# Kernel optimization log

Measured on AMD Instinct MI355X. Metric: run time of the kernel, lower is better.

## Reference

```python
import jax, jax.numpy as jnp
import numpy as np

N = 50000      # nodes
E = 800000     # edges (before self-loops)
F_IN = 128     # num_features
HID = 32       # hidden_channels
HEADS = 4
CLS = 40       # num_classes
NEG_SLOPE = 0.2


def setup_inputs() -> dict:
    key = jax.random.key(0)
    ks = jax.random.split(key, 10)
    s = 0.1
    x = jax.random.normal(ks[0], (N, F_IN), jnp.float32)
    edge_index = jax.random.randint(ks[1], (2, E), 0, N, jnp.int32)
    W1 = jax.random.normal(ks[2], (F_IN, HEADS * HID), jnp.float32) * s
    att_src1 = jax.random.normal(ks[3], (HEADS, HID), jnp.float32) * s
    att_dst1 = jax.random.normal(ks[4], (HEADS, HID), jnp.float32) * s
    b1 = jnp.zeros((HEADS * HID,), jnp.float32)
    W2 = jax.random.normal(ks[5], (HEADS * HID, CLS), jnp.float32) * s
    att_src2 = jax.random.normal(ks[6], (1, CLS), jnp.float32) * s
    att_dst2 = jax.random.normal(ks[7], (1, CLS), jnp.float32) * s
    b2 = jnp.zeros((CLS,), jnp.float32)
    return {"x": x, "edge_index": edge_index,
            "W1": W1, "att_src1": att_src1, "att_dst1": att_dst1, "b1": b1,
            "W2": W2, "att_src2": att_src2, "att_dst2": att_dst2, "b2": b2}


def gat_layer(x, src, dst, W, a_src, a_dst, b, concat):
    """PyG GATConv: per-head linear, edge attention logits a_src.h_j + a_dst.h_i,
    LeakyReLU, segment softmax over incoming edges per dst, weighted scatter-sum."""
    n = x.shape[0]
    H, C = a_src.shape
    h = (x @ W).reshape(n, H, C)                       # [N, H, C]
    al_s = jnp.einsum('nhc,hc->nh', h, a_src)          # [N, H]
    al_d = jnp.einsum('nhc,hc->nh', h, a_dst)          # [N, H]
    e = jax.nn.leaky_relu(al_s[src] + al_d[dst], NEG_SLOPE)  # [E, H]
    e_max = jax.lax.stop_gradient(jax.ops.segment_max(e, dst, num_segments=n))
    e = jnp.exp(e - e_max[dst])
    denom = jax.ops.segment_sum(e, dst, num_segments=n)      # [N, H]
    alpha = e / (denom[dst] + 1e-16)                         # [E, H]
    out = jax.ops.segment_sum(h[src] * alpha[:, :, None], dst, num_segments=n)  # [N, H, C]
    out = out.reshape(n, H * C) if concat else out.mean(axis=1)
    return out + b


def reference(x, edge_index, W1, att_src1, att_dst1, b1, W2, att_src2, att_dst2, b2):
    n = x.shape[0]
    loops = jnp.arange(n, dtype=edge_index.dtype)
    src = jnp.concatenate([edge_index[0], loops])  # PyG adds self-loops by default
    dst = jnp.concatenate([edge_index[1], loops])
    h = gat_layer(x, src, dst, W1, att_src1, att_dst1, b1, concat=True)
    h = jax.nn.relu(h)  # dropout is identity in eval mode
    h = gat_layer(h, src, dst, W2, att_src2, att_dst2, b2, concat=False)
    return jax.nn.log_softmax(h, axis=1)
```

## Files before the change

kernel.cpp:

```cpp
#include <hip/hip_runtime.h>
#include <hip/hip_bf16.h>
#include <cstdint>
#include <cstddef>

#define NN 50000
#define EE 800000
#define ETOT (EE + NN)
#define FIN 128
#define D1 128
#define HEADS 4
#define HID 32
#define CLS 40
#define NEG 0.2f
#define MAXDEG 64
#define NPART 8
#define PSIZE 6250
#define GB 104

typedef __attribute__((ext_vector_type(8))) short short8;
typedef __attribute__((ext_vector_type(4))) float float4v;

union U16 { uint4 u; short8 s; };

__device__ __forceinline__ float bf2f(unsigned short u) {
    union { unsigned int i; float f; } v; v.i = ((unsigned int)u) << 16; return v.f;
}
__device__ __forceinline__ unsigned short f2bf(float f) {
    union { unsigned int i; float f; } v; v.f = f;
    unsigned int r = v.i + 0x7fffu + ((v.i >> 16) & 1u);
    return (unsigned short)(r >> 16);
}

__global__ __launch_bounds__(256) void build_k(const int* __restrict__ eidx,
                                               int* __restrict__ cnt,
                                               unsigned short* __restrict__ ssrcp) {
    int part = blockIdx.x & (NPART - 1);
    int g    = blockIdx.x >> 3;
    int lo = part * PSIZE, hi = lo + PSIZE;
    int stride = GB * 256;
    for (int t = g * 256 + (int)threadIdx.x; t < ETOT; t += stride) {
        int dN = (t < EE) ? eidx[EE + t] : (t - EE);
        if (dN >= lo && dN < hi) {
            int sN = (t < EE) ? eidx[t] : dN;
            int slot = atomicAdd(&cnt[dN], 1);
            if (slot < MAXDEG) ssrcp[dN * MAXDEG + slot] = (unsigned short)sN;
        }
    }
}

__global__ __launch_bounds__(256) void gemm1_k(const float* __restrict__ X,
                                               const float* __restrict__ W,
                                               unsigned int* __restrict__ H1b) {
    __shared__ uint4 Wl[2048];
    int t = threadIdx.x;
    for (int g = t; g < 2048; g += 256) {
        int ct = g >> 8, rem = g & 255, kc = rem >> 6, l = rem & 63;
        int c = ct * 16 + (l & 15);
        int k0 = kc * 32 + (l >> 4) * 8;
        U16 u;
#pragma unroll
        for (int j = 0; j < 8; j++) u.s[j] = (short)f2bf(W[(k0 + j) * D1 + c]);
        Wl[g] = u.u;
    }
    __syncthreads();

    int wid = t >> 6, lane = t & 63, quad = lane >> 4, lrow = lane & 15;
    int wrow0 = blockIdx.x * 128 + wid * 32;

    short8 afr[2][4];
#pragma unroll
    for (int rt = 0; rt < 2; rt++) {
        int r = wrow0 + rt * 16 + lrow;
#pragma unroll
        for (int kc = 0; kc < 4; kc++) {
            short8 a = {0, 0, 0, 0, 0, 0, 0, 0};
            if (r < NN) {
                const float* xp = X + (size_t)r * FIN + kc * 32 + quad * 8;
                float4 x0 = *(const float4*)xp;
                float4 x1 = *(const float4*)(xp + 4);
                a[0] = (short)f2bf(x0.x); a[1] = (short)f2bf(x0.y);
                a[2] = (short)f2bf(x0.z); a[3] = (short)f2bf(x0.w);
                a[4] = (short)f2bf(x1.x); a[5] = (short)f2bf(x1.y);
                a[6] = (short)f2bf(x1.z); a[7] = (short)f2bf(x1.w);
            }
            afr[rt][kc] = a;
        }
    }

    float4v acc[2][8];
#pragma unroll
    for (int rt = 0; rt < 2; rt++)
#pragma unroll
        for (int ct = 0; ct < 8; ct++) acc[rt][ct] = (float4v)(0.f);

#pragma unroll
    for (int ct = 0; ct < 8; ct++) {
#pragma unroll
        for (int kc = 0; kc < 4; kc++) {
            U16 b; b.u = Wl[(ct * 4 + kc) * 64 + lane];
            acc[0][ct] = __builtin_amdgcn_mfma_f32_16x16x32_bf16(afr[0][kc], b.s, acc[0][ct], 0, 0, 0);
            acc[1][ct] = __builtin_amdgcn_mfma_f32_16x16x32_bf16(afr[1][kc], b.s, acc[1][ct], 0, 0, 0);
        }
    }

#pragma unroll
    for (int rt = 0; rt < 2; rt++)
#pragma unroll
        for (int ct = 0; ct < 8; ct++)
#pragma unroll
            for (int reg = 0; reg < 4; reg++) {
                float v = acc[rt][ct][reg];
                float o = __shfl_xor(v, 1);
                int r = wrow0 + rt * 16 + quad * 4 + reg;
                if (((lane & 1) == 0) && r < NN) {
                    unsigned int u = (unsigned int)f2bf(v) | ((unsigned int)f2bf(o) << 16);
                    H1b[(size_t)r * 64 + ct * 8 + (lrow >> 1)] = u;
                }
            }
}

__global__ void att1_k(const unsigned int* __restrict__ H1b,
                       const float* __restrict__ a_s, const float* __restrict__ a_d,
                       float* __restrict__ ALS, float* __restrict__ ALD) {
    int t = blockIdx.x * blockDim.x + threadIdx.x;
    if (t >= NN * HEADS) return;
    int n = t >> 2, h = t & 3;
    const unsigned int* row = H1b + (size_t)n * 64 + h * 16;
    float as = 0.f, ad = 0.f;
#pragma unroll
    for (int i = 0; i < 16; i++) {
        unsigned int u = row[i];
        float c0 = bf2f((unsigned short)(u & 0xffffu));
        float c1 = bf2f((unsigned short)(u >> 16));
        as += c0 * a_s[h * HID + 2 * i] + c1 * a_s[h * HID + 2 * i + 1];
        ad += c0 * a_d[h * HID + 2 * i] + c1 * a_d[h * HID + 2 * i + 1];
    }
    ALS[t] = as; ALD[t] = ad;
}

__global__ __launch_bounds__(128) void gather1_k(const int* __restrict__ cnt,
                                                 const unsigned short* __restrict__ ssrcp,
                                                 const unsigned int* __restrict__ H1b,
                                                 const float4* __restrict__ ALS,
                                                 const float4* __restrict__ ALD,
                                                 const float* __restrict__ b1,
                                                 unsigned int* __restrict__ OUT1b) {
    int v = blockIdx.x;
    int t = threadIdx.x;
    int deg = min(cnt[v], MAXDEG);
    __shared__ float w[MAXDEG][4];
    __shared__ int sid[MAXDEG];
    __shared__ float part[4][D1];
    __shared__ float sden[4];
    float4 ad = ALD[v];
    if (t < deg) {
        int s = (int)ssrcp[v * MAXDEG + t];
        sid[t] = s;
        float4 as = ALS[s];
        float l0 = as.x + ad.x; l0 = l0 > 0.f ? l0 : NEG * l0;
        float l1 = as.y + ad.y; l1 = l1 > 0.f ? l1 : NEG * l1;
        float l2 = as.z + ad.z; l2 = l2 > 0.f ? l2 : NEG * l2;
        float l3 = as.w + ad.w; l3 = l3 > 0.f ? l3 : NEG * l3;
        w[t][0] = __expf(l0); w[t][1] = __expf(l1);
        w[t][2] = __expf(l2); w[t][3] = __expf(l3);
    }
    __syncthreads();
    if (t < 4) {
        float d = 0.f;
        for (int j = 0; j < deg; j++) d += w[j][t];
        sden[t] = d;
    }
    int g = t >> 5, c = t & 31;
    int head = c >> 3;
    float4 acc = make_float4(0.f, 0.f, 0.f, 0.f);
    for (int j = g; j < deg; j += 4) {
        float wj = w[j][head];
        uint2 u = ((const uint2*)(H1b + (size_t)sid[j] * 64))[c];
        acc.x += wj * bf2f((unsigned short)(u.x & 0xffffu));
        acc.y += wj * bf2f((unsigned short)(u.x >> 16));
        acc.z += wj * bf2f((unsigned short)(u.y & 0xffffu));
        acc.w += wj * bf2f((unsigned short)(u.y >> 16));
    }
    *(float4*)&part[g][4 * c] = acc;
    __syncthreads();
    float o = (part[0][t] + part[1][t] + part[2][t] + part[3][t])
              / (sden[t >> 5] + 1e-16f) + b1[t];
    o = fmaxf(o, 0.f);
    float po = __shfl_xor(o, 1);
    if ((t & 1) == 0) {
        unsigned int u = (unsigned int)f2bf(o) | ((unsigned int)f2bf(po) << 16);
        OUT1b[(size_t)v * 64 + (t >> 1)] = u;
    }
}

__global__ __launch_bounds__(256) void gemm2_k(const unsigned int* __restrict__ OUT1b,
                                               const float* __restrict__ W2,
                                               unsigned int* __restrict__ H2b) {
    __shared__ uint4 Wl[768];
    int t = threadIdx.x;
    for (int g = t; g < 768; g += 256) {
        int ct = g >> 8, rem = g & 255, kc = rem >> 6, l = rem & 63;
        int c = ct * 16 + (l & 15);
        int k0 = kc * 32 + (l >> 4) * 8;
        U16 u;
#pragma unroll
        for (int j = 0; j < 8; j++)
            u.s[j] = (c < CLS) ? (short)f2bf(W2[(k0 + j) * CLS + c]) : (short)0;
        Wl[g] = u.u;
    }
    __syncthreads();

    int wid = t >> 6, lane = t & 63, quad = lane >> 4, lrow = lane & 15;
    int wrow0 = blockIdx.x * 128 + wid * 32;

    U16 afr[2][4];
#pragma unroll
    for (int rt = 0; rt < 2; rt++) {
        int r = wrow0 + rt * 16 + lrow;
#pragma unroll
        for (int kc = 0; kc < 4; kc++) {
            if (r < NN)
                afr[rt][kc].u = ((const uint4*)OUT1b)[(size_t)r * 16 + kc * 4 + quad];
            else
                afr[rt][kc].u = make_uint4(0, 0, 0, 0);
        }
    }

    float4v acc[2][3];
#pragma unroll
    for (int rt = 0; rt < 2; rt++)
#pragma unroll
        for (int ct = 0; ct < 3; ct++) acc[rt][ct] = (float4v)(0.f);

#pragma unroll
    for (int ct = 0; ct < 3; ct++) {
#pragma unroll
        for (int kc = 0; kc < 4; kc++) {
            U16 b; b.u = Wl[(ct * 4 + kc) * 64 + lane];
            acc[0][ct] = __builtin_amdgcn_mfma_f32_16x16x32_bf16(afr[0][kc].s, b.s, acc[0][ct], 0, 0, 0);
            acc[1][ct] = __builtin_amdgcn_mfma_f32_16x16x32_bf16(afr[1][kc].s, b.s, acc[1][ct], 0, 0, 0);
        }
    }

#pragma unroll
    for (int rt = 0; rt < 2; rt++)
#pragma unroll
        for (int ct = 0; ct < 3; ct++)
#pragma unroll
            for (int reg = 0; reg < 4; reg++) {
                float v = acc[rt][ct][reg];
                float o = __shfl_xor(v, 1);
                int r = wrow0 + rt * 16 + quad * 4 + reg;
                int c = ct * 16 + lrow;
                if (((lane & 1) == 0) && c < CLS && r < NN) {
                    unsigned int u = (unsigned int)f2bf(v) | ((unsigned int)f2bf(o) << 16);
                    H2b[(size_t)r * 20 + (c >> 1)] = u;
                }
            }
}

__global__ void att2_k(const unsigned int* __restrict__ H2b, const float* __restrict__ a_s,
                       const float* __restrict__ a_d,
                       float* __restrict__ ALS, float* __restrict__ ALD) {
    int n = blockIdx.x * blockDim.x + threadIdx.x;
    if (n >= NN) return;
    const unsigned int* row = H2b + (size_t)n * 20;
    float as = 0.f, ad = 0.f;
#pragma unroll
    for (int i = 0; i < 20; i++) {
        unsigned int u = row[i];
        float c0 = bf2f((unsigned short)(u & 0xffffu));
        float c1 = bf2f((unsigned short)(u >> 16));
        as += c0 * a_s[2 * i] + c1 * a_s[2 * i + 1];
        ad += c0 * a_d[2 * i] + c1 * a_d[2 * i + 1];
    }
    ALS[n] = as; ALD[n] = ad;
}

__global__ __launch_bounds__(64) void gather2_k(const int* __restrict__ cnt,
                                                const unsigned short* __restrict__ ssrcp,
                                                const unsigned int* __restrict__ H2b,
                                                const float* __restrict__ ALS,
                                                const float* __restrict__ ALD,
                                                const float* __restrict__ b2,
                                                float* __restrict__ out) {
    int v = blockIdx.x, t = threadIdx.x;
    int deg = min(cnt[v], MAXDEG);
    __shared__ float w[MAXDEG];
    __shared__ int sid[MAXDEG];
    __shared__ float part[2][CLS];
    float den = 0.f;
    float adv = ALD[v];
    if (t < deg) {
        int s = (int)ssrcp[v * MAXDEG + t];
        sid[t] = s;
        float l = ALS[s] + adv; l = l > 0.f ? l : NEG * l;
        float e = __expf(l);
        w[t] = e; den = e;
    }
    __syncthreads();
    int g = t >> 5, c = t & 31;
    if (c < 20) {
        float ax = 0.f, ay = 0.f;
        for (int j = g; j < deg; j += 2) {
            float wj = w[j];
            unsigned int u = H2b[(size_t)sid[j] * 20 + c];
            ax += wj * bf2f((unsigned short)(u & 0xffffu));
            ay += wj * bf2f((unsigned short)(u >> 16));
        }
        part[g][2 * c] = ax;
        part[g][2 * c + 1] = ay;
    }
#pragma unroll
    for (int o = 32; o > 0; o >>= 1) den += __shfl_xor(den, o);
    __syncthreads();
    float z = (t < CLS) ? (part[0][t] + part[1][t]) / (den + 1e-16f) + b2[t] : -1e30f;
    float mx = z;
#pragma unroll
    for (int o = 32; o > 0; o >>= 1) mx = fmaxf(mx, __shfl_xor(mx, o));
    float ex = (t < CLS) ? __expf(z - mx) : 0.f;
    float se = ex;
#pragma unroll
    for (int o = 32; o > 0; o >>= 1) se += __shfl_xor(se, o);
    if (t < CLS) out[(size_t)v * CLS + t] = z - mx - __logf(se);
}

extern "C" void kernel_launch(void* const* d_in, const int* in_sizes, int n_in,
                              void* d_out, int out_size, void* d_ws, size_t ws_size,
                              hipStream_t stream) {
    const float* x   = (const float*)d_in[0];
    const int*   eix = (const int*)d_in[1];
    const float* W1  = (const float*)d_in[2];
    const float* as1 = (const float*)d_in[3];
    const float* ad1 = (const float*)d_in[4];
    const float* b1  = (const float*)d_in[5];
    const float* W2  = (const float*)d_in[6];
    const float* as2 = (const float*)d_in[7];
    const float* ad2 = (const float*)d_in[8];
    const float* b2  = (const float*)d_in[9];
    float* out = (float*)d_out;

    char* p = (char*)d_ws;
    auto carve = [&](size_t bytes) -> void* {
        void* r = (void*)p;
        p += (bytes + 255) & ~(size_t)255;
        return r;
    };
    unsigned int* H1b   = (unsigned int*)carve((size_t)NN * 64 * 4);
    unsigned int* OUT1b = (unsigned int*)carve((size_t)NN * 64 * 4);
    unsigned int* H2b   = (unsigned int*)carve((size_t)NN * 20 * 4);
    float* ALS1 = (float*)carve((size_t)NN * 4 * 4);
    float* ALD1 = (float*)carve((size_t)NN * 4 * 4);
    float* ALS2 = (float*)carve((size_t)NN * 4);
    float* ALD2 = (float*)carve((size_t)NN * 4);
    int* cnt    = (int*)carve((size_t)NN * 4);
    unsigned short* ssrcp = (unsigned short*)carve((size_t)NN * MAXDEG * 2);

    hipMemsetAsync(cnt, 0, (size_t)NN * 4, stream);
    build_k<<<NPART * GB, 256, 0, stream>>>(eix, cnt, ssrcp);

    gemm1_k<<<(NN + 127) / 128, 256, 0, stream>>>(x, W1, H1b);
    att1_k<<<(NN * HEADS + 255) / 256, 256, 0, stream>>>(H1b, as1, ad1, ALS1, ALD1);
    gather1_k<<<NN, 128, 0, stream>>>(cnt, ssrcp, H1b, (const float4*)ALS1,
                                      (const float4*)ALD1, b1, OUT1b);

    gemm2_k<<<(NN + 127) / 128, 256, 0, stream>>>(OUT1b, W2, H2b);
    att2_k<<<(NN + 255) / 256, 256, 0, stream>>>(H2b, as2, ad2, ALS2, ALD2);
    gather2_k<<<NN, 64, 0, stream>>>(cnt, ssrcp, H2b, ALS2, ALD2, b2, out);
}
```

Measured before the change: 248.7 us.

## Fuse attention-logit dot products into GEMM epilogues and widen gather1 loads

Folds the per-node attention dot products (a_src·h, a_dst·h) for both layers into the MFMA GEMM epilogues. They are now reduced from the fp32 accumulators with lane shuffles instead of being computed by separate att1/att2 kernels that re-read H1b/H2b. This removes two kernel launches and their memory re-reads. Separately, gather1 now loads 16-byte uint4 rows with 8 edge groups of 16 lanes instead of 8-byte loads with 4 groups, and uses a padded partial-sum buffer. The logits now come from fp32 accumulators rather than bf16-rounded values, which changes numerics slightly.

Result: faster. 237.9 us (-4.4%).

```diff
diff --git a/kernel.cpp b/kernel.cpp
--- a/kernel.cpp
+++ b/kernel.cpp
@@ -50,9 +50,15 @@
 
 __global__ __launch_bounds__(256) void gemm1_k(const float* __restrict__ X,
                                                const float* __restrict__ W,
-                                               unsigned int* __restrict__ H1b) {
+                                               const float* __restrict__ as1,
+                                               const float* __restrict__ ad1,
+                                               unsigned int* __restrict__ H1b,
+                                               float* __restrict__ ALS1,
+                                               float* __restrict__ ALD1) {
     __shared__ uint4 Wl[2048];
+    __shared__ float sas[128], sad[128];
     int t = threadIdx.x;
+    if (t < 128) { sas[t] = as1[t]; sad[t] = ad1[t]; }
     for (int g = t; g < 2048; g += 256) {
         int ct = g >> 8, rem = g & 255, kc = rem >> 6, l = rem & 63;
         int c = ct * 16 + (l & 15);
@@ -104,6 +110,34 @@
     }
 
 #pragma unroll
+    for (int rt = 0; rt < 2; rt++) {
+#pragma unroll
+        for (int reg = 0; reg < 4; reg++) {
+            float ps[4] = {0.f, 0.f, 0.f, 0.f};
+            float pd[4] = {0.f, 0.f, 0.f, 0.f};
+#pragma unroll
+            for (int ct = 0; ct < 8; ct++) {
+                float v = acc[rt][ct][reg];
+                ps[ct >> 1] += v * sas[ct * 16 + lrow];
+                pd[ct >> 1] += v * sad[ct * 16 + lrow];
+            }
+#pragma unroll
+            for (int o = 1; o < 16; o <<= 1) {
+#pragma unroll
+                for (int h = 0; h < 4; h++) {
+                    ps[h] += __shfl_xor(ps[h], o);
+                    pd[h] += __shfl_xor(pd[h], o);
+                }
+            }
+            int r = wrow0 + rt * 16 + quad * 4 + reg;
+            if (lrow == 0 && r < NN) {
+                *(float4*)&ALS1[(size_t)r * 4] = make_float4(ps[0], ps[1], ps[2], ps[3]);
+                *(float4*)&ALD1[(size_t)r * 4] = make_float4(pd[0], pd[1], pd[2], pd[3]);
+            }
+        }
+    }
+
+#pragma unroll
     for (int rt = 0; rt < 2; rt++)
 #pragma unroll
         for (int ct = 0; ct < 8; ct++)
@@ -119,28 +153,9 @@
             }
 }
 
-__global__ void att1_k(const unsigned int* __restrict__ H1b,
-                       const float* __restrict__ a_s, const float* __restrict__ a_d,
-                       float* __restrict__ ALS, float* __restrict__ ALD) {
-    int t = blockIdx.x * blockDim.x + threadIdx.x;
-    if (t >= NN * HEADS) return;
-    int n = t >> 2, h = t & 3;
-    const unsigned int* row = H1b + (size_t)n * 64 + h * 16;
-    float as = 0.f, ad = 0.f;
-#pragma unroll
-    for (int i = 0; i < 16; i++) {
-        unsigned int u = row[i];
-        float c0 = bf2f((unsigned short)(u & 0xffffu));
-        float c1 = bf2f((unsigned short)(u >> 16));
-        as += c0 * a_s[h * HID + 2 * i] + c1 * a_s[h * HID + 2 * i + 1];
-        ad += c0 * a_d[h * HID + 2 * i] + c1 * a_d[h * HID + 2 * i + 1];
-    }
-    ALS[t] = as; ALD[t] = ad;
-}
-
 __global__ __launch_bounds__(128) void gather1_k(const int* __restrict__ cnt,
                                                  const unsigned short* __restrict__ ssrcp,
-                                                 const unsigned int* __restrict__ H1b,
+                                                 const uint4* __restrict__ H1b4,
                                                  const float4* __restrict__ ALS,
                                                  const float4* __restrict__ ALD,
                                                  const float* __restrict__ b1,
@@ -150,7 +165,7 @@
     int deg = min(cnt[v], MAXDEG);
     __shared__ float w[MAXDEG][4];
     __shared__ int sid[MAXDEG];
-    __shared__ float part[4][D1];
+    __shared__ float part[8][132];
     __shared__ float sden[4];
     float4 ad = ALD[v];
     if (t < deg) {
@@ -170,34 +185,49 @@
         for (int j = 0; j < deg; j++) d += w[j][t];
         sden[t] = d;
     }
-    int g = t >> 5, c = t & 31;
-    int head = c >> 3;
-    float4 acc = make_float4(0.f, 0.f, 0.f, 0.f);
-    for (int j = g; j < deg; j += 4) {
+    int u = t >> 4, l = t & 15;
+    int head = l >> 2;
+    float a0=0.f,a1=0.f,a2=0.f,a3=0.f,a4=0.f,a5=0.f,a6=0.f,a7=0.f;
+    for (int j = u; j < deg; j += 8) {
         float wj = w[j][head];
-        uint2 u = ((const uint2*)(H1b + (size_t)sid[j] * 64))[c];
-        acc.x += wj * bf2f((unsigned short)(u.x & 0xffffu));
-        acc.y += wj * bf2f((unsigned short)(u.x >> 16));
-        acc.z += wj * bf2f((unsigned short)(u.y & 0xffffu));
-        acc.w += wj * bf2f((unsigned short)(u.y >> 16));
-    }
-    *(float4*)&part[g][4 * c] = acc;
-    __syncthreads();
-    float o = (part[0][t] + part[1][t] + part[2][t] + part[3][t])
+        uint4 q = H1b4[(size_t)sid[j] * 16 + l];
+        a0 += wj * bf2f((unsigned short)(q.x & 0xffffu));
+        a1 += wj * bf2f((unsigned short)(q.x >> 16));
+        a2 += wj * bf2f((unsigned short)(q.y & 0xffffu));
+        a3 += wj * bf2f((unsigned short)(q.y >> 16));
+        a4 += wj * bf2f((unsigned short)(q.z & 0xffffu));
+        a5 += wj * bf2f((unsigned short)(q.z >> 16));
+        a6 += wj * bf2f((unsigned short)(q.w & 0xffffu));
+        a7 += wj * bf2f((unsigned short)(q.w >> 16));
+    }
+    float* pp = &part[u][8 * l];
+    pp[0]=a0; pp[1]=a1; pp[2]=a2; pp[3]=a3; pp[4]=a4; pp[5]=a5; pp[6]=a6; pp[7]=a7;
+    __syncthreads();
+    float o = (part[0][t] + part[1][t] + part[2][t] + part[3][t] +
+               part[4][t] + part[5][t] + part[6][t] + part[7][t])
               / (sden[t >> 5] + 1e-16f) + b1[t];
     o = fmaxf(o, 0.f);
     float po = __shfl_xor(o, 1);
     if ((t & 1) == 0) {
-        unsigned int u = (unsigned int)f2bf(o) | ((unsigned int)f2bf(po) << 16);
-        OUT1b[(size_t)v * 64 + (t >> 1)] = u;
+        unsigned int uu = (unsigned int)f2bf(o) | ((unsigned int)f2bf(po) << 16);
+        OUT1b[(size_t)v * 64 + (t >> 1)] = uu;
     }
 }
 
 __global__ __launch_bounds__(256) void gemm2_k(const unsigned int* __restrict__ OUT1b,
                                                const float* __restrict__ W2,
-                                               unsigned int* __restrict__ H2b) {
+                                               const float* __restrict__ as2,
+                                               const float* __restrict__ ad2,
+                                               unsigned int* __restrict__ H2b,
+                                               float* __restrict__ ALS2,
+                                               float* __restrict__ ALD2) {
     __shared__ uint4 Wl[768];
+    __shared__ float sas[48], sad[48];
     int t = threadIdx.x;
+    if (t < 48) {
+        sas[t] = (t < CLS) ? as2[t] : 0.f;
+        sad[t] = (t < CLS) ? ad2[t] : 0.f;
+    }
     for (int g = t; g < 768; g += 256) {
         int ct = g >> 8, rem = g & 255, kc = rem >> 6, l = rem & 63;
         int c = ct * 16 + (l & 15);
@@ -239,6 +269,30 @@
             U16 b; b.u = Wl[(ct * 4 + kc) * 64 + lane];
             acc[0][ct] = __builtin_amdgcn_mfma_f32_16x16x32_bf16(afr[0][kc].s, b.s, acc[0][ct], 0, 0, 0);
             acc[1][ct] = __builtin_amdgcn_mfma_f32_16x16x32_bf16(afr[1][kc].s, b.s, acc[1][ct], 0, 0, 0);
+        }
+    }
+
+#pragma unroll
+    for (int rt = 0; rt < 2; rt++) {
+#pragma unroll
+        for (int reg = 0; reg < 4; reg++) {
+            float ps = 0.f, pd = 0.f;
+#pragma unroll
+            for (int ct = 0; ct < 3; ct++) {
+                float v = acc[rt][ct][reg];
+                ps += v * sas[ct * 16 + lrow];
+                pd += v * sad[ct * 16 + lrow];
+            }
+#pragma unroll
+            for (int o = 1; o < 16; o <<= 1) {
+                ps += __shfl_xor(ps, o);
+                pd += __shfl_xor(pd, o);
+            }
+            int r = wrow0 + rt * 16 + quad * 4 + reg;
+            if (lrow == 0 && r < NN) {
+                ALS2[r] = ps;
+                ALD2[r] = pd;
+            }
         }
     }
 
@@ -257,24 +311,6 @@
                     H2b[(size_t)r * 20 + (c >> 1)] = u;
                 }
             }
-}
-
-__global__ void att2_k(const unsigned int* __restrict__ H2b, const float* __restrict__ a_s,
-                       const float* __restrict__ a_d,
-                       float* __restrict__ ALS, float* __restrict__ ALD) {
-    int n = blockIdx.x * blockDim.x + threadIdx.x;
-    if (n >= NN) return;
-    const unsigned int* row = H2b + (size_t)n * 20;
-    float as = 0.f, ad = 0.f;
-#pragma unroll
-    for (int i = 0; i < 20; i++) {
-        unsigned int u = row[i];
-        float c0 = bf2f((unsigned short)(u & 0xffffu));
-        float c1 = bf2f((unsigned short)(u >> 16));
-        as += c0 * a_s[2 * i] + c1 * a_s[2 * i + 1];
-        ad += c0 * a_d[2 * i] + c1 * a_d[2 * i + 1];
-    }
-    ALS[n] = as; ALD[n] = ad;
 }
 
 __global__ __launch_bounds__(64) void gather2_k(const int* __restrict__ cnt,
@@ -359,12 +395,10 @@
     hipMemsetAsync(cnt, 0, (size_t)NN * 4, stream);
     build_k<<<NPART * GB, 256, 0, stream>>>(eix, cnt, ssrcp);
 
-    gemm1_k<<<(NN + 127) / 128, 256, 0, stream>>>(x, W1, H1b);
-    att1_k<<<(NN * HEADS + 255) / 256, 256, 0, stream>>>(H1b, as1, ad1, ALS1, ALD1);
-    gather1_k<<<NN, 128, 0, stream>>>(cnt, ssrcp, H1b, (const float4*)ALS1,
+    gemm1_k<<<(NN + 127) / 128, 256, 0, stream>>>(x, W1, as1, ad1, H1b, ALS1, ALD1);
+    gather1_k<<<NN, 128, 0, stream>>>(cnt, ssrcp, (const uint4*)H1b, (const float4*)ALS1,
                                       (const float4*)ALD1, b1, OUT1b);
 
-    gemm2_k<<<(NN + 127) / 128, 256, 0, stream>>>(OUT1b, W2, H2b);
-    att2_k<<<(NN + 255) / 256, 256, 0, stream>>>(H2b, as2, ad2, ALS2, ALD2);
+    gemm2_k<<<(NN + 127) / 128, 256, 0, stream>>>(OUT1b, W2, as2, ad2, H2b, ALS2, ALD2);
     gather2_k<<<NN, 64, 0, stream>>>(cnt, ssrcp, H2b, ALS2, ALD2, b2, out);
 }
```
